# Optimization experiments

Hardware: AMD Instinct MI355X
Metric: run time of the kernel (lower is better)

Reference implementation:

```python
import jax, jax.numpy as jnp
import numpy as np

# init_kwargs (density_alpha=0 -> density weight == 1.0 for every image)
COUNT_W = 2.5
SPATIAL_W = 0.1
SCALE_W = 0.3  # multiplies a constant-zero scale_loss, kept for fidelity

B, H, W = 64, 512, 512
N_PTS = 512
H_IN = W_IN = 2048


def setup_inputs() -> dict:
    key = jax.random.key(0)
    k1, k2 = jax.random.split(key)
    pred = jax.random.uniform(k1, (B, 1, H, W), dtype=jnp.float32)  # raw density
    # point coordinates (x, y) in input-image pixel space [0, 2048)
    points = jax.random.uniform(k2, (B, N_PTS, 2), dtype=jnp.float32) * float(W_IN)
    return {"pred": pred, "points": points, "cell_area": 16, "H_in": H_IN, "W_in": W_IN}


def reference(pred, points, cell_area, H_in, W_in):
    Bb, _, Hh, Ww = pred.shape
    n = points.shape[1]  # gt count per image (padded-uniform point list)

    # ---- count loss (MAE on counts; density weight = 1 since alpha = 0) ----
    pred_counts = pred.sum(axis=(1, 2, 3)) / cell_area            # [B]
    count_loss = jnp.abs(pred_counts - n).sum() / Bb

    # ---- gaussian-splat target (vectorized scatter-add over B*N*9) ----
    scale_h = Hh / H_in
    scale_w = Ww / W_in
    # torch: int(clamp(pt * scale, 0, dim-1)) -> clip then truncate (coords >= 0)
    x = jnp.clip(points[..., 0] * scale_w, 0, Ww - 1).astype(jnp.int32)  # [B,N]
    y = jnp.clip(points[..., 1] * scale_h, 0, Hh - 1).astype(jnp.int32)  # [B,N]

    offs = jnp.array([(dy, dx) for dy in (-1, 0, 1) for dx in (-1, 0, 1)],
                     dtype=jnp.int32)                              # [9,2]
    wgt = jnp.exp(-jnp.sqrt(jnp.sum(offs.astype(jnp.float32) ** 2, -1)) / 2.0)  # [9]

    ny = y[..., None] + offs[:, 0]                                 # [B,N,9]
    nx = x[..., None] + offs[:, 1]                                 # [B,N,9]
    valid = (ny >= 0) & (ny < Hh) & (nx >= 0) & (nx < Ww)
    wv = jnp.where(valid, wgt, 0.0)                                # [B,N,9]

    bidx = jnp.arange(Bb)[:, None, None]
    target = jnp.zeros((Bb, Hh, Ww), pred.dtype).at[
        bidx, jnp.clip(ny, 0, Hh - 1), jnp.clip(nx, 0, Ww - 1)
    ].add(wv)                                                      # [B,H,W]

    # ---- spatial loss: MSE between normalized density maps ----
    tsum = target.sum(axis=(1, 2), keepdims=True)                  # > 0 always (n > 0)
    target = target / tsum
    p = pred[:, 0]
    pred_norm = p / (p.sum(axis=(1, 2), keepdims=True) + 1e-8)
    spatial_loss = jnp.mean((pred_norm - target) ** 2, axis=(1, 2)).sum() / Bb

    scale_loss = jnp.zeros((), pred.dtype)
    total = COUNT_W * count_loss + SPATIAL_W * spatial_loss + SCALE_W * scale_loss
    return total, count_loss, spatial_loss
```

## Files before the change

### kernel.cpp

```cpp
#include <hip/hip_runtime.h>

#define NB     64
#define HH     512
#define WW     512
#define HWSZ   (HH * WW)
#define NPTS   512
#define RBPB   4
#define NRB    (NB * RBPB)
#define HSLOTS 8192

__device__ __forceinline__ float waveReduceSum(float v) {
    for (int o = 32; o > 0; o >>= 1) v += __shfl_down(v, o);
    return v;
}

__global__ __launch_bounds__(512)
void k_fused(const float* __restrict__ pred, const float* __restrict__ points,
             const int* __restrict__ pHin, const int* __restrict__ pWin,
             float* __restrict__ Spart, float* __restrict__ P2part,
             float* __restrict__ T2, float* __restrict__ DOT, float* __restrict__ TS) {
    __shared__ unsigned keys[HSLOTS];
    __shared__ float    vals[HSLOTS];
    const int tid = threadIdx.x;

    if (blockIdx.x >= NB) {
        const int rb = blockIdx.x - NB;
        const float4* base = (const float4*)pred + (size_t)rb * (HWSZ / RBPB / 4);
        float s = 0.f, q = 0.f;
#pragma unroll
        for (int i = 0; i < 32; ++i) {
            float4 v = base[tid + i * 512];
            s += (v.x + v.y) + (v.z + v.w);
            q += v.x * v.x + v.y * v.y + v.z * v.z + v.w * v.w;
        }
        s = waveReduceSum(s);
        q = waveReduceSum(q);
        const int wave = tid >> 6, lane = tid & 63;
        if (lane == 0) { vals[wave] = s; vals[8 + wave] = q; }
        __syncthreads();
        if (tid == 0) {
            float a = 0.f, b2 = 0.f;
            for (int w = 0; w < 8; ++w) { a += vals[w]; b2 += vals[8 + w]; }
            Spart[rb] = a; P2part[rb] = b2;
        }
        return;
    }

    const int b = blockIdx.x;
    for (int i = tid; i < HSLOTS; i += 512) { keys[i] = 0xFFFFFFFFu; vals[i] = 0.f; }
    __syncthreads();

    const float scale_w = (float)WW / (float)(*pWin);
    const float scale_h = (float)HH / (float)(*pHin);
    const float wEdge = expf(-0.5f);
    const float wDiag = expf(-0.70710678118654752440f);

    float wsum = 0.f;
    {
        const float2 pt = ((const float2*)points)[(size_t)b * NPTS + tid];
        int x = (int)fminf(fmaxf(pt.x * scale_w, 0.f), (float)(WW - 1));
        int y = (int)fminf(fmaxf(pt.y * scale_h, 0.f), (float)(HH - 1));
#pragma unroll
        for (int dy = -1; dy <= 1; ++dy)
#pragma unroll
            for (int dx = -1; dx <= 1; ++dx) {
                int ny = y + dy, nx = x + dx;
                if (ny < 0 || ny >= HH || nx < 0 || nx >= WW) continue;
                int d2 = dy * dy + dx * dx;
                float w = (d2 == 0) ? 1.f : ((d2 == 1) ? wEdge : wDiag);
                wsum += w;
                unsigned key = (unsigned)(ny * WW + nx);
                unsigned h = (key * 2654435761u) >> 19;
                for (;;) {
                    unsigned old = atomicCAS(&keys[h], 0xFFFFFFFFu, key);
                    if (old == 0xFFFFFFFFu || old == key) { atomicAdd(&vals[h], w); break; }
                    h = (h + 1) & (HSLOTS - 1);
                }
            }
    }
    __syncthreads();

    float t2 = 0.f, dot = 0.f;
    const float* pb = pred + (size_t)b * HWSZ;
    for (int i = tid; i < HSLOTS; i += 512) {
        unsigned key = keys[i];
        if (key != 0xFFFFFFFFu) {
            float t = vals[i];
            t2  += t * t;
            dot += t * pb[key];
        }
    }

    wsum = waveReduceSum(wsum);
    t2   = waveReduceSum(t2);
    dot  = waveReduceSum(dot);
    __syncthreads();
    const int wave = tid >> 6, lane = tid & 63;
    if (lane == 0) { vals[wave] = wsum; vals[8 + wave] = t2; vals[16 + wave] = dot; }
    __syncthreads();
    if (tid == 0) {
        float a0 = 0.f, a1 = 0.f, a2 = 0.f;
        for (int w = 0; w < 8; ++w) { a0 += vals[w]; a1 += vals[8 + w]; a2 += vals[16 + w]; }
        TS[b] = a0; T2[b] = a1; DOT[b] = a2;
    }
}

__global__ __launch_bounds__(64)
void k_final(const float* __restrict__ Spart, const float* __restrict__ P2part,
             const float* __restrict__ T2, const float* __restrict__ DOT,
             const float* __restrict__ TS, const int* __restrict__ pCell,
             float* __restrict__ out) {
    int t = threadIdx.x;
    double cl = 0.0, sl = 0.0;
    if (t < NB) {
        double s = 0.0, p2 = 0.0;
#pragma unroll
        for (int c = 0; c < RBPB; ++c) {
            s  += (double)Spart[t * RBPB + c];
            p2 += (double)P2part[t * RBPB + c];
        }
        cl = fabs(s / (double)(*pCell) - (double)NPTS);
        double sn = s + 1e-8;
        double ts = (double)TS[t];
        double term = p2 / (sn * sn)
                    - 2.0 * (double)DOT[t] / (sn * ts)
                    + (double)T2[t] / (ts * ts);
        sl = term / (double)HWSZ;
    }
    for (int o = 32; o > 0; o >>= 1) { cl += __shfl_down(cl, o); sl += __shfl_down(sl, o); }
    if (t == 0) {
        double count_loss   = cl / (double)NB;
        double spatial_loss = sl / (double)NB;
        double total = 2.5 * count_loss + 0.1 * spatial_loss;
        out[0] = (float)total;
        out[1] = (float)count_loss;
        out[2] = (float)spatial_loss;
    }
}

extern "C" void kernel_launch(void* const* d_in, const int* in_sizes, int n_in,
                              void* d_out, int out_size, void* d_ws, size_t ws_size,
                              hipStream_t stream) {
    const float* pred   = (const float*)d_in[0];
    const float* points = (const float*)d_in[1];
    const int*   cell   = (const int*)d_in[2];
    const int*   hin    = (const int*)d_in[3];
    const int*   win    = (const int*)d_in[4];
    float* out = (float*)d_out;

    float* Spart  = (float*)d_ws;
    float* P2part = Spart + NRB;
    float* T2     = Spart + 2 * NRB;
    float* DOT    = T2 + NB;
    float* TS     = DOT + NB;

    k_fused<<<NB + NRB, 512, 0, stream>>>(pred, points, hin, win,
                                          Spart, P2part, T2, DOT, TS);
    k_final<<<1, 64, 0, stream>>>(Spart, P2part, T2, DOT, TS, cell, out);
}
```

Measured before the change: 111.8 us.

## Replace shared-memory hash splat with pairwise point-overlap algebra for target terms

Drops the LDS hash table with atomicCAS probing. sum(t^2) is now computed as a sum over point pairs of a precomputed 5x5 kernel-overlap table, with an explicit fallback for points near the border. The dot product is taken directly per point from pred. This removes 64KB of LDS per block, which should allow higher occupancy, and removes the atomic contention. In exchange each thread does an O(N^2) scan over 512 shared coordinates. The reduction blocks per image also go from 4 to 8, each with a manually unrolled batch of 8 loads.

Result: slower. 154.0 us (+37.7%).

```diff
diff --git a/kernel.cpp b/kernel.cpp
--- a/kernel.cpp
+++ b/kernel.cpp
@@ -5,9 +5,9 @@
 #define WW     512
 #define HWSZ   (HH * WW)
 #define NPTS   512
-#define RBPB   4
+#define RBPB   8
 #define NRB    (NB * RBPB)
-#define HSLOTS 8192
+#define NBLK   (NB + NRB)
 
 __device__ __forceinline__ float waveReduceSum(float v) {
     for (int o = 32; o > 0; o >>= 1) v += __shfl_down(v, o);
@@ -15,12 +15,13 @@
 }
 
 __global__ __launch_bounds__(512)
-void k_fused(const float* __restrict__ pred, const float* __restrict__ points,
-             const int* __restrict__ pHin, const int* __restrict__ pWin,
-             float* __restrict__ Spart, float* __restrict__ P2part,
-             float* __restrict__ T2, float* __restrict__ DOT, float* __restrict__ TS) {
-    __shared__ unsigned keys[HSLOTS];
-    __shared__ float    vals[HSLOTS];
+void k_main(const float* __restrict__ pred, const float* __restrict__ points,
+            const int* __restrict__ pHin, const int* __restrict__ pWin,
+            float* __restrict__ Spart, float* __restrict__ P2part,
+            float* __restrict__ T2, float* __restrict__ DOT, float* __restrict__ TS) {
+    __shared__ int   xs[NPTS], ys[NPTS];
+    __shared__ float T5[25];
+    __shared__ float red[24];
     const int tid = threadIdx.x;
 
     if (blockIdx.x >= NB) {
@@ -28,89 +29,123 @@
         const float4* base = (const float4*)pred + (size_t)rb * (HWSZ / RBPB / 4);
         float s = 0.f, q = 0.f;
 #pragma unroll
-        for (int i = 0; i < 32; ++i) {
-            float4 v = base[tid + i * 512];
-            s += (v.x + v.y) + (v.z + v.w);
-            q += v.x * v.x + v.y * v.y + v.z * v.z + v.w * v.w;
+        for (int it = 0; it < 2; ++it) {
+            float4 v0 = base[tid + (it * 8 + 0) * 512];
+            float4 v1 = base[tid + (it * 8 + 1) * 512];
+            float4 v2 = base[tid + (it * 8 + 2) * 512];
+            float4 v3 = base[tid + (it * 8 + 3) * 512];
+            float4 v4 = base[tid + (it * 8 + 4) * 512];
+            float4 v5 = base[tid + (it * 8 + 5) * 512];
+            float4 v6 = base[tid + (it * 8 + 6) * 512];
+            float4 v7 = base[tid + (it * 8 + 7) * 512];
+            s += (v0.x + v0.y) + (v0.z + v0.w);  q += v0.x*v0.x + v0.y*v0.y + v0.z*v0.z + v0.w*v0.w;
+            s += (v1.x + v1.y) + (v1.z + v1.w);  q += v1.x*v1.x + v1.y*v1.y + v1.z*v1.z + v1.w*v1.w;
+            s += (v2.x + v2.y) + (v2.z + v2.w);  q += v2.x*v2.x + v2.y*v2.y + v2.z*v2.z + v2.w*v2.w;
+            s += (v3.x + v3.y) + (v3.z + v3.w);  q += v3.x*v3.x + v3.y*v3.y + v3.z*v3.z + v3.w*v3.w;
+            s += (v4.x + v4.y) + (v4.z + v4.w);  q += v4.x*v4.x + v4.y*v4.y + v4.z*v4.z + v4.w*v4.w;
+            s += (v5.x + v5.y) + (v5.z + v5.w);  q += v5.x*v5.x + v5.y*v5.y + v5.z*v5.z + v5.w*v5.w;
+            s += (v6.x + v6.y) + (v6.z + v6.w);  q += v6.x*v6.x + v6.y*v6.y + v6.z*v6.z + v6.w*v6.w;
+            s += (v7.x + v7.y) + (v7.z + v7.w);  q += v7.x*v7.x + v7.y*v7.y + v7.z*v7.z + v7.w*v7.w;
         }
         s = waveReduceSum(s);
         q = waveReduceSum(q);
         const int wave = tid >> 6, lane = tid & 63;
-        if (lane == 0) { vals[wave] = s; vals[8 + wave] = q; }
+        if (lane == 0) { red[wave] = s; red[8 + wave] = q; }
         __syncthreads();
         if (tid == 0) {
             float a = 0.f, b2 = 0.f;
-            for (int w = 0; w < 8; ++w) { a += vals[w]; b2 += vals[8 + w]; }
+            for (int w = 0; w < 8; ++w) { a += red[w]; b2 += red[8 + w]; }
             Spart[rb] = a; P2part[rb] = b2;
         }
         return;
     }
 
     const int b = blockIdx.x;
-    for (int i = tid; i < HSLOTS; i += 512) { keys[i] = 0xFFFFFFFFu; vals[i] = 0.f; }
+    const float scale_w = (float)WW / (float)(*pWin);
+    const float scale_h = (float)HH / (float)(*pHin);
+    const float wE = expf(-0.5f);
+    const float wD = expf(-0.70710678118654752440f);
+
+    if (tid < 25) {
+        int dY = tid / 5 - 2, dX = tid % 5 - 2;
+        float acc = 0.f;
+        for (int dyi = -1; dyi <= 1; ++dyi)
+            for (int dxi = -1; dxi <= 1; ++dxi) {
+                int dyj = dyi - dY, dxj = dxi - dX;
+                if (dyj < -1 || dyj > 1 || dxj < -1 || dxj > 1) continue;
+                int d2i = dyi * dyi + dxi * dxi;
+                int d2j = dyj * dyj + dxj * dxj;
+                float wi = (d2i == 0) ? 1.f : ((d2i == 1) ? wE : wD);
+                float wj = (d2j == 0) ? 1.f : ((d2j == 1) ? wE : wD);
+                acc += wi * wj;
+            }
+        T5[tid] = acc;
+    }
+
+    const float2 pt = ((const float2*)points)[(size_t)b * NPTS + tid];
+    const int xi = (int)fminf(fmaxf(pt.x * scale_w, 0.f), (float)(WW - 1));
+    const int yi = (int)fminf(fmaxf(pt.y * scale_h, 0.f), (float)(HH - 1));
+    xs[tid] = xi; ys[tid] = yi;
+
+    const float* pb = pred + (size_t)b * HWSZ;
+    float wsum = 0.f, dot = 0.f;
+#pragma unroll
+    for (int dy = -1; dy <= 1; ++dy)
+#pragma unroll
+        for (int dx = -1; dx <= 1; ++dx) {
+            int ny = yi + dy, nx = xi + dx;
+            if (ny < 0 || ny >= HH || nx < 0 || nx >= WW) continue;
+            int d2 = dy * dy + dx * dx;
+            float w = (d2 == 0) ? 1.f : ((d2 == 1) ? wE : wD);
+            wsum += w;
+            dot  += w * pb[ny * WW + nx];
+        }
     __syncthreads();
 
-    const float scale_w = (float)WW / (float)(*pWin);
-    const float scale_h = (float)HH / (float)(*pHin);
-    const float wEdge = expf(-0.5f);
-    const float wDiag = expf(-0.70710678118654752440f);
-
-    float wsum = 0.f;
-    {
-        const float2 pt = ((const float2*)points)[(size_t)b * NPTS + tid];
-        int x = (int)fminf(fmaxf(pt.x * scale_w, 0.f), (float)(WW - 1));
-        int y = (int)fminf(fmaxf(pt.y * scale_h, 0.f), (float)(HH - 1));
-#pragma unroll
-        for (int dy = -1; dy <= 1; ++dy)
-#pragma unroll
-            for (int dx = -1; dx <= 1; ++dx) {
-                int ny = y + dy, nx = x + dx;
-                if (ny < 0 || ny >= HH || nx < 0 || nx >= WW) continue;
-                int d2 = dy * dy + dx * dx;
-                float w = (d2 == 0) ? 1.f : ((d2 == 1) ? wEdge : wDiag);
-                wsum += w;
-                unsigned key = (unsigned)(ny * WW + nx);
-                unsigned h = (key * 2654435761u) >> 19;
-                for (;;) {
-                    unsigned old = atomicCAS(&keys[h], 0xFFFFFFFFu, key);
-                    if (old == 0xFFFFFFFFu || old == key) { atomicAdd(&vals[h], w); break; }
-                    h = (h + 1) & (HSLOTS - 1);
+    const bool ii = (xi >= 1) & (xi <= WW - 2) & (yi >= 1) & (yi <= HH - 2);
+    float t2 = 0.f;
+    for (int j = 0; j < NPTS; ++j) {
+        int xj = xs[j], yj = ys[j];
+        int dX = xj - xi, dY = yj - yi;
+        if ((unsigned)(dX + 2) > 4u || (unsigned)(dY + 2) > 4u) continue;
+        bool ij = (xj >= 1) & (xj <= WW - 2) & (yj >= 1) & (yj <= HH - 2);
+        if (ii & ij) {
+            t2 += T5[(dY + 2) * 5 + (dX + 2)];
+        } else {
+            for (int dyi = -1; dyi <= 1; ++dyi)
+                for (int dxi = -1; dxi <= 1; ++dxi) {
+                    int cy = yi + dyi, cx = xi + dxi;
+                    if (cy < 0 || cy >= HH || cx < 0 || cx >= WW) continue;
+                    int dyj = dyi - dY, dxj = dxi - dX;
+                    if (dyj < -1 || dyj > 1 || dxj < -1 || dxj > 1) continue;
+                    int d2i = dyi * dyi + dxi * dxi;
+                    int d2j = dyj * dyj + dxj * dxj;
+                    float wi = (d2i == 0) ? 1.f : ((d2i == 1) ? wE : wD);
+                    float wj = (d2j == 0) ? 1.f : ((d2j == 1) ? wE : wD);
+                    t2 += wi * wj;
                 }
-            }
-    }
-    __syncthreads();
-
-    float t2 = 0.f, dot = 0.f;
-    const float* pb = pred + (size_t)b * HWSZ;
-    for (int i = tid; i < HSLOTS; i += 512) {
-        unsigned key = keys[i];
-        if (key != 0xFFFFFFFFu) {
-            float t = vals[i];
-            t2  += t * t;
-            dot += t * pb[key];
         }
     }
 
     wsum = waveReduceSum(wsum);
     t2   = waveReduceSum(t2);
     dot  = waveReduceSum(dot);
-    __syncthreads();
     const int wave = tid >> 6, lane = tid & 63;
-    if (lane == 0) { vals[wave] = wsum; vals[8 + wave] = t2; vals[16 + wave] = dot; }
+    if (lane == 0) { red[wave] = wsum; red[8 + wave] = t2; red[16 + wave] = dot; }
     __syncthreads();
     if (tid == 0) {
         float a0 = 0.f, a1 = 0.f, a2 = 0.f;
-        for (int w = 0; w < 8; ++w) { a0 += vals[w]; a1 += vals[8 + w]; a2 += vals[16 + w]; }
+        for (int w = 0; w < 8; ++w) { a0 += red[w]; a1 += red[8 + w]; a2 += red[16 + w]; }
         TS[b] = a0; T2[b] = a1; DOT[b] = a2;
     }
 }
 
 __global__ __launch_bounds__(64)
-void k_final(const float* __restrict__ Spart, const float* __restrict__ P2part,
-             const float* __restrict__ T2, const float* __restrict__ DOT,
-             const float* __restrict__ TS, const int* __restrict__ pCell,
-             float* __restrict__ out) {
-    int t = threadIdx.x;
+void k_fin(const float* __restrict__ Spart, const float* __restrict__ P2part,
+           const float* __restrict__ T2, const float* __restrict__ DOT,
+           const float* __restrict__ TS, const int* __restrict__ pCell,
+           float* __restrict__ out) {
+    const int t = threadIdx.x;
     double cl = 0.0, sl = 0.0;
     if (t < NB) {
         double s = 0.0, p2 = 0.0;
@@ -154,7 +189,7 @@
     float* DOT    = T2 + NB;
     float* TS     = DOT + NB;
 
-    k_fused<<<NB + NRB, 512, 0, stream>>>(pred, points, hin, win,
-                                          Spart, P2part, T2, DOT, TS);
-    k_final<<<1, 64, 0, stream>>>(Spart, P2part, T2, DOT, TS, cell, out);
+    k_main<<<NBLK, 512, 0, stream>>>(pred, points, hin, win,
+                                     Spart, P2part, T2, DOT, TS);
+    k_fin<<<1, 64, 0, stream>>>(Spart, P2part, T2, DOT, TS, cell, out);
 }
```
